# Kernel optimization log

Hardware: AMD Instinct MI355X
Metric: run time of the kernel (lower is better)

Reference implementation:

```python
import jax, jax.numpy as jnp
import numpy as np


def apply_rope(t, seq_len, d_head):
    # t: [B, H, S, d_head]; interleaved-pair RoPE matching the torch module
    inv_freq = 1.0 / (10000.0 ** (jnp.arange(0, d_head, 2, dtype=jnp.float32) / d_head))
    angles = jnp.arange(seq_len, dtype=jnp.float32)[:, None] * inv_freq[None, :]  # [S, d/2]
    sin = jnp.sin(angles)[None, None, :, :, None]  # broadcast over B, H, pair
    cos = jnp.cos(angles)[None, None, :, :, None]
    tr = t.reshape(*t.shape[:-1], -1, 2)  # [B, H, S, d/2, 2]
    rot = jnp.stack([-tr[..., 1], tr[..., 0]], axis=-1)
    out = tr * cos + rot * sin
    return out.reshape(t.shape)


def setup_inputs() -> dict:
    key = jax.random.key(0)
    ks = jax.random.split(key, 10)
    B, S, D, L = 8, 4096, 1024, 64
    s = 0.02
    return {
        "x": jax.random.normal(ks[0], (B, S, D), dtype=jnp.float32),
        "latents": jax.random.normal(ks[1], (L, D), dtype=jnp.float32),
        "q_w": jax.random.normal(ks[2], (D, D), dtype=jnp.float32) * s,
        "q_b": jax.random.normal(ks[3], (D,), dtype=jnp.float32) * s,
        "k_w": jax.random.normal(ks[4], (D, D), dtype=jnp.float32) * s,
        "k_b": jax.random.normal(ks[5], (D,), dtype=jnp.float32) * s,
        "v_w": jax.random.normal(ks[6], (D, D), dtype=jnp.float32) * s,
        "v_b": jax.random.normal(ks[7], (D,), dtype=jnp.float32) * s,
        "out_w": jax.random.normal(ks[8], (D, D), dtype=jnp.float32) * s,
        "out_b": jax.random.normal(ks[9], (D,), dtype=jnp.float32) * s,
    }


def reference(x, latents, q_w, q_b, k_w, k_b, v_w, v_b, out_w, out_b):
    B, S, D = x.shape
    H = 16
    dh = D // H
    L = latents.shape[0]

    # latent queries (shared across batch)
    lq = latents @ q_w.T + q_b                      # [L, D]
    lq = jnp.broadcast_to(lq[None], (B, L, D))
    k = x @ k_w.T + k_b                             # [B, S, D]
    v = x @ v_w.T + v_b

    lq = lq.reshape(B, L, H, dh).transpose(0, 2, 1, 3)   # [B, H, L, dh]
    k = k.reshape(B, S, H, dh).transpose(0, 2, 1, 3)     # [B, H, S, dh]
    v = v.reshape(B, S, H, dh).transpose(0, 2, 1, 3)

    lq = apply_rope(lq, L, dh)
    k = apply_rope(k, S, dh)

    scores = jnp.einsum('bhld,bhsd->bhls', lq, k) / jnp.sqrt(jnp.float32(dh))
    attn = jax.nn.softmax(scores, axis=-1)
    out = jnp.einsum('bhls,bhsd->bhld', attn, v)          # [B, H, L, dh]
    out = out.transpose(0, 2, 1, 3).reshape(B, L, D)
    return out @ out_w.T + out_b
```

## Files before the change

kernel.cpp:

```cpp
#include <hip/hip_runtime.h>
#include <hip/hip_bf16.h>
#include <math.h>


typedef __attribute__((ext_vector_type(8))) short bf16x8;
typedef __attribute__((ext_vector_type(4))) float f32x4;

#define MFMA16(a, b, c) __builtin_amdgcn_mfma_f32_16x16x32_bf16((a), (b), (c), 0, 0, 0)

__device__ __forceinline__ unsigned short f2bf(float f) {
  unsigned int u = __float_as_uint(f);
  u = (u + 0x7fffu + ((u >> 16) & 1u)) >> 16;
  return (unsigned short)u;
}

__device__ __forceinline__ void gload_lds16(const void* g, void* l) {
  __builtin_amdgcn_global_load_lds((const __attribute__((address_space(1))) void*)g,
                                   (__attribute__((address_space(3))) void*)l,
                                   16, 0, 0);
}

__global__ __launch_bounds__(256) void cast_f32_bf16(const float* __restrict__ in,
                                                     unsigned short* __restrict__ out,
                                                     int n4) {
  int i = blockIdx.x * 256 + threadIdx.x;
  const int stride = gridDim.x * 256;
  for (; i < n4; i += stride) {
    const float4 v = ((const float4*)in)[i];
    ushort4 o;
    o.x = f2bf(v.x); o.y = f2bf(v.y); o.z = f2bf(v.z); o.w = f2bf(v.w);
    ((ushort4*)out)[i] = o;
  }
}

__global__ __launch_bounds__(256) void rope_table_kernel(float2* __restrict__ cs) {
  const int id = blockIdx.x * 256 + threadIdx.x;
  const int s = id >> 5, p = id & 31;
  const float inv = (float)pow(10000.0, -(double)(2 * p) / 64.0);
  const float ang = (float)s * inv;
  cs[id] = make_float2(cosf(ang), sinf(ang));
}

__global__ __launch_bounds__(256) void lq_mfma_kernel(
    const unsigned short* __restrict__ latbf, const unsigned short* __restrict__ qwbf,
    const float* __restrict__ qb, const float2* __restrict__ cs,
    unsigned short* __restrict__ lqbf) {
  __shared__ unsigned short As[64 * 64];
  __shared__ unsigned short Bs[128 * 64];
  const int tid = threadIdx.x;
  const int lane = tid & 63, w = tid >> 6;
  const int cl = lane & 15, g8 = (lane >> 4) * 8, g4 = (lane >> 4) * 4;
  const int n0 = (int)blockIdx.x * 128;
  f32x4 acc[4][2] = {};
  for (int ks = 0; ks < 16; ++ks) {
    const int k0 = ks * 64;
    if (ks) __syncthreads();
#pragma unroll
    for (int i = 0; i < 2; ++i) {
      const int e = i * 2048 + tid * 8;
      gload_lds16(latbf + (size_t)(e >> 6) * 1024 + k0 + (e & 63), &As[i * 2048 + w * 512]);
    }
#pragma unroll
    for (int i = 0; i < 4; ++i) {
      const int e = i * 2048 + tid * 8;
      gload_lds16(qwbf + (size_t)(n0 + (e >> 6)) * 1024 + k0 + (e & 63), &Bs[i * 2048 + w * 512]);
    }
    __syncthreads();
#pragma unroll
    for (int kk = 0; kk < 2; ++kk) {
      bf16x8 af[4], bfr[2];
#pragma unroll
      for (int t = 0; t < 4; ++t)
        af[t] = *(const bf16x8*)&As[(t * 16 + cl) * 64 + kk * 32 + g8];
#pragma unroll
      for (int t = 0; t < 2; ++t)
        bfr[t] = *(const bf16x8*)&Bs[(w * 32 + t * 16 + cl) * 64 + kk * 32 + g8];
#pragma unroll
      for (int i = 0; i < 4; ++i)
#pragma unroll
        for (int j = 0; j < 2; ++j)
          acc[i][j] = MFMA16(af[i], bfr[j], acc[i][j]);
    }
  }
#pragma unroll
  for (int i = 0; i < 4; ++i)
#pragma unroll
    for (int j = 0; j < 2; ++j) {
      const int colg = n0 + w * 32 + j * 16 + cl;
      const float bv = qb[colg];
      const int p = (colg & 63) >> 1;
#pragma unroll
      for (int r = 0; r < 4; ++r) {
        const int l = i * 16 + g4 + r;
        float v = acc[i][j][r] + bv;
        const float2 c2 = cs[l * 32 + p];
        const float other = __shfl_xor(v, 1);
        v = (colg & 1) ? fmaf(v, c2.x, other * c2.y) : fmaf(v, c2.x, -other * c2.y);
        lqbf[l * 1024 + colg] = f2bf(v * 0.125f);
      }
    }
}

__global__ __launch_bounds__(256) void kv_proj_kernel(
    const unsigned short* __restrict__ xbf,
    const unsigned short* __restrict__ kwbf, const unsigned short* __restrict__ vwbf,
    const float* __restrict__ kb, const float* __restrict__ vb,
    const float2* __restrict__ cs,
    unsigned short* __restrict__ Kbf, unsigned short* __restrict__ Vbf) {
  __shared__ unsigned short As[128 * 64];
  __shared__ unsigned short Bs[128 * 64];
  const int tid = threadIdx.x;
  const int lane = tid & 63;
  const int w = tid >> 6;
  const int wr = w >> 1, wc = w & 1;
  const int cl = lane & 15, g8 = (lane >> 4) * 8, g4 = (lane >> 4) * 4;
  const int bid = (int)blockIdx.x;
  const int swz = (bid & 7) * 512 + (bid >> 3);
  const int m0 = (swz >> 4) * 128;
  const int n0 = (swz & 15) * 128;
  const bool isK = n0 < 1024;
  const unsigned short* wbf = isK ? kwbf : vwbf;
  const int nl = isK ? n0 : n0 - 1024;
  const int ldsb = w * 512;

  f32x4 acc[4][4] = {};

  for (int ks = 0; ks < 16; ++ks) {
    const int k0 = ks * 64;
    if (ks) __syncthreads();
#pragma unroll
    for (int i = 0; i < 4; ++i) {
      const int e = i * 2048 + tid * 8;
      const int row = e >> 6, col = e & 63;
      gload_lds16(xbf + (size_t)(m0 + row) * 1024 + k0 + col, &As[i * 2048 + ldsb]);
    }
#pragma unroll
    for (int i = 0; i < 4; ++i) {
      const int e = i * 2048 + tid * 8;
      const int row = e >> 6, col = e & 63;
      gload_lds16(wbf + (size_t)(nl + row) * 1024 + k0 + col, &Bs[i * 2048 + ldsb]);
    }
    __syncthreads();
#pragma unroll
    for (int kk = 0; kk < 2; ++kk) {
      bf16x8 af[4], bfr[4];
#pragma unroll
      for (int t = 0; t < 4; ++t)
        af[t] = *(const bf16x8*)&As[(wr * 64 + t * 16 + cl) * 64 + kk * 32 + g8];
#pragma unroll
      for (int t = 0; t < 4; ++t)
        bfr[t] = *(const bf16x8*)&Bs[(wc * 64 + t * 16 + cl) * 64 + kk * 32 + g8];
#pragma unroll
      for (int i = 0; i < 4; ++i)
#pragma unroll
        for (int j = 0; j < 4; ++j)
          acc[i][j] = MFMA16(af[i], bfr[j], acc[i][j]);
    }
  }

  const float* bias = isK ? kb : vb;
  unsigned short* outp = isK ? Kbf : Vbf;
#pragma unroll
  for (int i = 0; i < 4; ++i) {
#pragma unroll
    for (int j = 0; j < 4; ++j) {
      const int colg = nl + wc * 64 + j * 16 + cl;
      const float bv = bias[colg];
#pragma unroll
      for (int r = 0; r < 4; ++r) {
        const int m = m0 + wr * 64 + i * 16 + g4 + r;
        float v = acc[i][j][r] + bv;
        if (isK) {
          const int s = m & 4095;
          const int p = (colg & 63) >> 1;
          const float2 c2 = cs[s * 32 + p];
          const float other = __shfl_xor(v, 1);
          v = (colg & 1) ? fmaf(v, c2.x, other * c2.y) : fmaf(v, c2.x, -other * c2.y);
        }
        outp[(size_t)m * 1024 + colg] = f2bf(v);
      }
    }
  }
}

__global__ __launch_bounds__(256) void attn_kernel(
    const unsigned short* __restrict__ lqbf,
    const unsigned short* __restrict__ Kbf, const unsigned short* __restrict__ Vbf,
    float* __restrict__ Opart, float* __restrict__ ml) {
  __shared__ unsigned short Qs[64 * 64];
  __shared__ unsigned short Ks[4][32 * 64];
  __shared__ unsigned short Vs[4][32 * 64];
  __shared__ unsigned short Pb[4][64 * 32];
  const int tid = threadIdx.x;
  const int w = tid >> 6, lane = tid & 63;
  const int cl = lane & 15, g = lane >> 4, g8 = g * 8, g4 = g * 4;
  const int gid = blockIdx.x;
  const int c = gid & 3;
  const int h = (gid >> 2) & 15;
  const int b = gid >> 6;

#pragma unroll
  for (int i = 0; i < 2; ++i) {
    const int e = i * 2048 + tid * 8;
    const int l = e >> 6, d = e & 63;
    *(uint4*)&Qs[e] = *(const uint4*)&lqbf[l * 1024 + h * 64 + d];
  }
  __syncthreads();
  bf16x8 qf[4][2];
#pragma unroll
  for (int li = 0; li < 4; ++li)
#pragma unroll
    for (int kk = 0; kk < 2; ++kk)
      qf[li][kk] = *(const bf16x8*)&Qs[(li * 16 + cl) * 64 + kk * 32 + g8];

  float m_r[4][4], l_r[4][4];
  f32x4 acc_o[4][4] = {};
#pragma unroll
  for (int li = 0; li < 4; ++li)
#pragma unroll
    for (int r = 0; r < 4; ++r) { m_r[li][r] = -INFINITY; l_r[li][r] = 0.f; }

  const size_t kvbase = ((size_t)(b * 4096)) * 1024 + h * 64;
  for (int t = 0; t < 8; ++t) {
    const int s0 = c * 1024 + t * 128 + w * 32;
#pragma unroll
    for (int i = 0; i < 4; ++i) {
      const int e = i * 512 + lane * 8;
      const int r = e >> 6, d = e & 63;
      const size_t ga = kvbase + (size_t)(s0 + r) * 1024 + d;
      *(uint4*)&Ks[w][e] = *(const uint4*)&Kbf[ga];
      *(uint4*)&Vs[w][e] = *(const uint4*)&Vbf[ga];
    }
    f32x4 sc[4][2] = {};
#pragma unroll
    for (int kk = 0; kk < 2; ++kk)
#pragma unroll
      for (int sj = 0; sj < 2; ++sj) {
        const bf16x8 kf = *(const bf16x8*)&Ks[w][(sj * 16 + cl) * 64 + kk * 32 + g8];
#pragma unroll
        for (int li = 0; li < 4; ++li)
          sc[li][sj] = MFMA16(qf[li][kk], kf, sc[li][sj]);
      }
#pragma unroll
    for (int li = 0; li < 4; ++li) {
#pragma unroll
      for (int r = 0; r < 4; ++r) {
        const float v0 = sc[li][0][r], v1 = sc[li][1][r];
        float mx = fmaxf(v0, v1);
        mx = fmaxf(mx, __shfl_xor(mx, 1));
        mx = fmaxf(mx, __shfl_xor(mx, 2));
        mx = fmaxf(mx, __shfl_xor(mx, 4));
        mx = fmaxf(mx, __shfl_xor(mx, 8));
        const float mo = m_r[li][r];
        const float nm = fmaxf(mo, mx);
        const float p0 = __expf(v0 - nm);
        const float p1 = __expf(v1 - nm);
        const float f = __expf(mo - nm);
        m_r[li][r] = nm;
        float sp = p0 + p1;
        sp += __shfl_xor(sp, 1);
        sp += __shfl_xor(sp, 2);
        sp += __shfl_xor(sp, 4);
        sp += __shfl_xor(sp, 8);
        l_r[li][r] = l_r[li][r] * f + sp;
#pragma unroll
        for (int di = 0; di < 4; ++di) acc_o[li][di][r] *= f;
        const int lrow = li * 16 + g4 + r;
        Pb[w][lrow * 32 + cl] = f2bf(p0);
        Pb[w][lrow * 32 + 16 + cl] = f2bf(p1);
      }
    }
    bf16x8 pa[4];
#pragma unroll
    for (int li = 0; li < 4; ++li)
      pa[li] = *(const bf16x8*)&Pb[w][(li * 16 + cl) * 32 + g8];
#pragma unroll
    for (int di = 0; di < 4; ++di) {
      bf16x8 bv;
#pragma unroll
      for (int e = 0; e < 8; ++e)
        bv[e] = (short)Vs[w][(g8 + e) * 64 + di * 16 + cl];
#pragma unroll
      for (int li = 0; li < 4; ++li)
        acc_o[li][di] = MFMA16(pa[li], bv, acc_o[li][di]);
    }
  }
  const int part = c * 4 + w;
  const size_t obase = (((size_t)(b * 16 + h)) * 16 + part) * 4096;
#pragma unroll
  for (int li = 0; li < 4; ++li)
#pragma unroll
    for (int di = 0; di < 4; ++di)
#pragma unroll
      for (int r = 0; r < 4; ++r)
        Opart[obase + (size_t)(li * 16 + g4 + r) * 64 + di * 16 + cl] = acc_o[li][di][r];
  if (cl == 0) {
    const size_t mb = (((size_t)(b * 16 + h)) * 16 + part) * 128;
#pragma unroll
    for (int li = 0; li < 4; ++li)
#pragma unroll
      for (int r = 0; r < 4; ++r) {
        ml[mb + li * 16 + g4 + r] = m_r[li][r];
        ml[mb + 64 + li * 16 + g4 + r] = l_r[li][r];
      }
  }
}

__global__ __launch_bounds__(256) void combine_kernel(
    const float* __restrict__ Opart, const float* __restrict__ ml,
    float* __restrict__ attn_out) {
  const int id = blockIdx.x * 256 + threadIdx.x;
  const int d = id & 63;
  const int l = (id >> 6) & 63;
  const int h = (id >> 12) & 15;
  const int b = id >> 16;
  const size_t bh = (size_t)(b * 16 + h);
  float M = -INFINITY;
#pragma unroll
  for (int p = 0; p < 16; ++p) M = fmaxf(M, ml[(bh * 16 + p) * 128 + l]);
  float t = 0.f, acc = 0.f;
#pragma unroll
  for (int p = 0; p < 16; ++p) {
    const float mp = ml[(bh * 16 + p) * 128 + l];
    const float lp = ml[(bh * 16 + p) * 128 + 64 + l];
    const float wgt = __expf(mp - M);
    t += lp * wgt;
    acc += wgt * Opart[(bh * 16 + p) * 4096 + l * 64 + d];
  }
  attn_out[((size_t)(b * 64 + l)) * 1024 + h * 64 + d] = acc / t;
}

__global__ __launch_bounds__(256) void out_proj_kernel(
    const float* __restrict__ A, const float* __restrict__ Wt,
    const float* __restrict__ bias, float* __restrict__ C) {
  __shared__ float As[32 * 33];
  __shared__ float Bs[64 * 33];
  const int tid = threadIdx.x;
  const int m0 = (int)(blockIdx.x & 15) * 32;
  const int n0 = (int)(blockIdx.x >> 4) * 64;
  const int r0 = (tid >> 4) * 2;
  const int c0 = (tid & 15) * 4;
  float acc[2][4] = {};
  for (int k0 = 0; k0 < 1024; k0 += 32) {
    if (k0) __syncthreads();
    {
      const int row = tid >> 3, col = (tid & 7) * 4;
      const float4 a4 = *(const float4*)&A[(size_t)(m0 + row) * 1024 + k0 + col];
      As[row * 33 + col] = a4.x; As[row * 33 + col + 1] = a4.y;
      As[row * 33 + col + 2] = a4.z; As[row * 33 + col + 3] = a4.w;
    }
#pragma unroll
    for (int i = 0; i < 2; ++i) {
      const int e = i * 1024 + tid * 4;
      const int row = e >> 5, col = e & 31;
      const float4 b4 = *(const float4*)&Wt[(size_t)(n0 + row) * 1024 + k0 + col];
      Bs[row * 33 + col] = b4.x; Bs[row * 33 + col + 1] = b4.y;
      Bs[row * 33 + col + 2] = b4.z; Bs[row * 33 + col + 3] = b4.w;
    }
    __syncthreads();
#pragma unroll
    for (int kk = 0; kk < 32; ++kk) {
      const float a0 = As[r0 * 33 + kk], a1 = As[(r0 + 1) * 33 + kk];
      float bv[4];
#pragma unroll
      for (int j = 0; j < 4; ++j) bv[j] = Bs[(c0 + j) * 33 + kk];
#pragma unroll
      for (int j = 0; j < 4; ++j) {
        acc[0][j] = fmaf(a0, bv[j], acc[0][j]);
        acc[1][j] = fmaf(a1, bv[j], acc[1][j]);
      }
    }
  }
#pragma unroll
  for (int i = 0; i < 2; ++i)
#pragma unroll
    for (int j = 0; j < 4; ++j)
      C[(size_t)(m0 + r0 + i) * 1024 + n0 + c0 + j] = acc[i][j] + bias[n0 + c0 + j];
}

extern "C" void kernel_launch(void* const* d_in, const int* in_sizes, int n_in,
                              void* d_out, int out_size, void* d_ws, size_t ws_size,
                              hipStream_t stream) {
  (void)in_sizes; (void)n_in; (void)out_size; (void)ws_size;
  const float* x = (const float*)d_in[0];
  const float* latents = (const float*)d_in[1];
  const float* q_w = (const float*)d_in[2];
  const float* q_b = (const float*)d_in[3];
  const float* k_w = (const float*)d_in[4];
  const float* k_b = (const float*)d_in[5];
  const float* v_w = (const float*)d_in[6];
  const float* v_b = (const float*)d_in[7];
  const float* out_w = (const float*)d_in[8];
  const float* out_b = (const float*)d_in[9];
  float* out = (float*)d_out;

  char* ws = (char*)d_ws;
  size_t off = 0;
  auto alloc = [&](size_t bytes) {
    char* p = ws + off;
    off += (bytes + 255) & ~(size_t)255;
    return p;
  };
  unsigned short* xbf   = (unsigned short*)alloc(33554432ull * 2);
  unsigned short* kwbf  = (unsigned short*)alloc(1048576ull * 2);
  unsigned short* vwbf  = (unsigned short*)alloc(1048576ull * 2);
  unsigned short* qwbf  = (unsigned short*)alloc(1048576ull * 2);
  unsigned short* latbf = (unsigned short*)alloc(65536ull * 2);
  unsigned short* lqbf  = (unsigned short*)alloc(65536ull * 2);
  float2*         cs    = (float2*)alloc(4096ull * 32 * 8);
  unsigned short* Kbf   = (unsigned short*)alloc(33554432ull * 2);
  unsigned short* Vbf   = (unsigned short*)alloc(33554432ull * 2);
  float*          Opart = (float*)alloc(8ull * 16 * 16 * 4096 * 4);
  float*          mlbuf = (float*)alloc(8ull * 16 * 16 * 128 * 4);
  float*          attn_out = (float*)alloc(512ull * 1024 * 4);

  cast_f32_bf16<<<2048, 256, 0, stream>>>(x, xbf, 33554432 / 4);
  cast_f32_bf16<<<512, 256, 0, stream>>>(k_w, kwbf, 1048576 / 4);
  cast_f32_bf16<<<512, 256, 0, stream>>>(v_w, vwbf, 1048576 / 4);
  cast_f32_bf16<<<512, 256, 0, stream>>>(q_w, qwbf, 1048576 / 4);
  cast_f32_bf16<<<64, 256, 0, stream>>>(latents, latbf, 65536 / 4);
  rope_table_kernel<<<512, 256, 0, stream>>>(cs);
  lq_mfma_kernel<<<8, 256, 0, stream>>>(latbf, qwbf, q_b, cs, lqbf);
  kv_proj_kernel<<<4096, 256, 0, stream>>>(xbf, kwbf, vwbf, k_b, v_b, cs, Kbf, Vbf);
  attn_kernel<<<512, 256, 0, stream>>>(lqbf, Kbf, Vbf, Opart, mlbuf);
  combine_kernel<<<2048, 256, 0, stream>>>(Opart, mlbuf, attn_out);
  out_proj_kernel<<<256, 256, 0, stream>>>(attn_out, out_w, out_b, out);
}
```

Before: 608.9 us.

## Rewrite KV projection GEMM with 256x256 tiles and double-buffered async LDS loads

After: 590.3 us. 3.1% less time.

```diff
diff --git a/kernel.cpp b/kernel.cpp
--- a/kernel.cpp
+++ b/kernel.cpp
@@ -36,7 +36,7 @@
 __global__ __launch_bounds__(256) void rope_table_kernel(float2* __restrict__ cs) {
   const int id = blockIdx.x * 256 + threadIdx.x;
   const int s = id >> 5, p = id & 31;
-  const float inv = (float)pow(10000.0, -(double)(2 * p) / 64.0);
+  const float inv = exp2f(-(float)p * 0.41524100875f);
   const float ang = (float)s * inv;
   cs[id] = make_float2(cosf(ang), sinf(ang));
 }
@@ -101,75 +101,104 @@
     }
 }
 
-__global__ __launch_bounds__(256) void kv_proj_kernel(
+__global__ __launch_bounds__(512, 2) void kv_proj_kernel(
     const unsigned short* __restrict__ xbf,
     const unsigned short* __restrict__ kwbf, const unsigned short* __restrict__ vwbf,
     const float* __restrict__ kb, const float* __restrict__ vb,
     const float2* __restrict__ cs,
     unsigned short* __restrict__ Kbf, unsigned short* __restrict__ Vbf) {
-  __shared__ unsigned short As[128 * 64];
-  __shared__ unsigned short Bs[128 * 64];
+  __shared__ unsigned short lds[2][4][8192];
   const int tid = threadIdx.x;
-  const int lane = tid & 63;
-  const int w = tid >> 6;
-  const int wr = w >> 1, wc = w & 1;
+  const int lane = tid & 63, w = tid >> 6;
+  const int wm = w >> 2, wn = w & 3;
   const int cl = lane & 15, g8 = (lane >> 4) * 8, g4 = (lane >> 4) * 4;
   const int bid = (int)blockIdx.x;
-  const int swz = (bid & 7) * 512 + (bid >> 3);
-  const int m0 = (swz >> 4) * 128;
-  const int n0 = (swz & 15) * 128;
+  const int swz = (bid & 7) * 128 + (bid >> 3);
+  const int m0 = (swz >> 3) * 256;
+  const int n0 = (swz & 7) * 256;
   const bool isK = n0 < 1024;
   const unsigned short* wbf = isK ? kwbf : vwbf;
   const int nl = isK ? n0 : n0 - 1024;
-  const int ldsb = w * 512;
-
-  f32x4 acc[4][4] = {};
-
-  for (int ks = 0; ks < 16; ++ks) {
-    const int k0 = ks * 64;
-    if (ks) __syncthreads();
-#pragma unroll
-    for (int i = 0; i < 4; ++i) {
-      const int e = i * 2048 + tid * 8;
-      const int row = e >> 6, col = e & 63;
-      gload_lds16(xbf + (size_t)(m0 + row) * 1024 + k0 + col, &As[i * 2048 + ldsb]);
-    }
-#pragma unroll
-    for (int i = 0; i < 4; ++i) {
-      const int e = i * 2048 + tid * 8;
-      const int row = e >> 6, col = e & 63;
-      gload_lds16(wbf + (size_t)(nl + row) * 1024 + k0 + col, &Bs[i * 2048 + ldsb]);
-    }
-    __syncthreads();
+
+  const int srow = tid >> 2;
+  const int sg8 = (tid & 3) * 8;
+  const unsigned short* srcA = xbf + (size_t)(m0 + srow) * 1024 + sg8;
+  const unsigned short* srcB = wbf + (size_t)(nl + srow) * 1024 + sg8;
+  const int ldso0 = w * 512;
+  const int ldso1 = 4096 + w * 512;
+
+#define STAGE_A(nb_, slot_, koff_) do {                                   \
+    gload_lds16(srcA + (koff_), &lds[nb_][slot_][ldso0]);                 \
+    gload_lds16(srcA + 131072 + (koff_), &lds[nb_][slot_][ldso1]); } while (0)
+#define STAGE_B(nb_, slot_, koff_) do {                                   \
+    gload_lds16(srcB + (koff_), &lds[nb_][slot_][ldso0]);                 \
+    gload_lds16(srcB + 131072 + (koff_), &lds[nb_][slot_][ldso1]); } while (0)
+
+  const int rdA = (wm * 128 + cl) * 32 + g8;
+  const int rdB = (wn * 64 + cl) * 32 + g8;
+
+  f32x4 acc[8][4] = {};
+
+  STAGE_A(0, 0, 0);
+  STAGE_B(0, 2, 0);
+  STAGE_A(0, 1, 32);
+  STAGE_B(0, 3, 32);
+
+#pragma unroll 2
+  for (int t = 0; t < 16; ++t) {
+    const int cb = t & 1, nb = cb ^ 1;
+    const int tn = (t < 15) ? t + 1 : 15;
+    const int kn = tn * 64;
 #pragma unroll
     for (int kk = 0; kk < 2; ++kk) {
-      bf16x8 af[4], bfr[4];
-#pragma unroll
-      for (int t = 0; t < 4; ++t)
-        af[t] = *(const bf16x8*)&As[(wr * 64 + t * 16 + cl) * 64 + kk * 32 + g8];
-#pragma unroll
-      for (int t = 0; t < 4; ++t)
-        bfr[t] = *(const bf16x8*)&Bs[(wc * 64 + t * 16 + cl) * 64 + kk * 32 + g8];
-#pragma unroll
-      for (int i = 0; i < 4; ++i)
-#pragma unroll
-        for (int j = 0; j < 4; ++j)
-          acc[i][j] = MFMA16(af[i], bfr[j], acc[i][j]);
-    }
-  }
+      asm volatile("s_waitcnt vmcnt(4)" ::: "memory");
+      __builtin_amdgcn_s_barrier();
+      asm volatile("" ::: "memory");
+      bf16x8 aF[4], bF[4];
+#pragma unroll
+      for (int x = 0; x < 4; ++x)
+        aF[x] = *(const bf16x8*)&lds[cb][kk][rdA + x * 512];
+#pragma unroll
+      for (int x = 0; x < 4; ++x)
+        bF[x] = *(const bf16x8*)&lds[cb][2 + kk][rdB + x * 512];
+      STAGE_A(nb, kk, kn + kk * 32);
+      __builtin_amdgcn_s_setprio(1);
+#pragma unroll
+      for (int mf = 0; mf < 4; ++mf)
+#pragma unroll
+        for (int nf = 0; nf < 4; ++nf)
+          acc[mf][nf] = MFMA16(aF[mf], bF[nf], acc[mf][nf]);
+      __builtin_amdgcn_s_setprio(0);
+      bf16x8 aG[4];
+#pragma unroll
+      for (int x = 0; x < 4; ++x)
+        aG[x] = *(const bf16x8*)&lds[cb][kk][rdA + (4 + x) * 512];
+      STAGE_B(nb, 2 + kk, kn + kk * 32);
+      __builtin_amdgcn_s_setprio(1);
+#pragma unroll
+      for (int mf = 0; mf < 4; ++mf)
+#pragma unroll
+        for (int nf = 0; nf < 4; ++nf)
+          acc[4 + mf][nf] = MFMA16(aG[mf], bF[nf], acc[4 + mf][nf]);
+      __builtin_amdgcn_s_setprio(0);
+    }
+  }
+  asm volatile("s_waitcnt vmcnt(0)" ::: "memory");
+#undef STAGE_A
+#undef STAGE_B
 
   const float* bias = isK ? kb : vb;
   unsigned short* outp = isK ? Kbf : Vbf;
 #pragma unroll
-  for (int i = 0; i < 4; ++i) {
-#pragma unroll
-    for (int j = 0; j < 4; ++j) {
-      const int colg = nl + wc * 64 + j * 16 + cl;
+  for (int mf = 0; mf < 8; ++mf) {
+#pragma unroll
+    for (int nf = 0; nf < 4; ++nf) {
+      const int colg = nl + wn * 64 + nf * 16 + cl;
       const float bv = bias[colg];
 #pragma unroll
       for (int r = 0; r < 4; ++r) {
-        const int m = m0 + wr * 64 + i * 16 + g4 + r;
-        float v = acc[i][j][r] + bv;
+        const int m = m0 + wm * 128 + mf * 16 + g4 + r;
+        float v = acc[mf][nf][r] + bv;
         if (isK) {
           const int s = m & 4095;
           const int p = (colg & 63) >> 1;
@@ -421,7 +450,7 @@
   cast_f32_bf16<<<64, 256, 0, stream>>>(latents, latbf, 65536 / 4);
   rope_table_kernel<<<512, 256, 0, stream>>>(cs);
   lq_mfma_kernel<<<8, 256, 0, stream>>>(latbf, qwbf, q_b, cs, lqbf);
-  kv_proj_kernel<<<4096, 256, 0, stream>>>(xbf, kwbf, vwbf, k_b, v_b, cs, Kbf, Vbf);
+  kv_proj_kernel<<<1024, 512, 0, stream>>>(xbf, kwbf, vwbf, k_b, v_b, cs, Kbf, Vbf);
   attn_kernel<<<512, 256, 0, stream>>>(lqbf, Kbf, Vbf, Opart, mlbuf);
   combine_kernel<<<2048, 256, 0, stream>>>(Opart, mlbuf, attn_out);
   out_proj_kernel<<<256, 256, 0, stream>>>(attn_out, out_w, out_b, out);
```
